# Kernel optimization log

Measured on AMD Instinct MI355X. Metric: run time of the kernel, lower is better.

Reference implementation:

```python
import jax, jax.numpy as jnp
import numpy as np

D_MODEL = 1024
NUM_HEADS = 16
HEAD_DIM = D_MODEL // NUM_HEADS
SCALE = HEAD_DIM ** -0.5


def setup_inputs() -> dict:
    key = jax.random.key(0)
    ks = jax.random.split(key, 8)
    B, Nq, Nk = 2, 2048, 2048
    s = D_MODEL ** -0.5  # init scale for weights
    return {
        "query": jax.random.normal(ks[0], (B, Nq, D_MODEL), jnp.float32),
        "key": jax.random.normal(ks[1], (B, Nk, D_MODEL), jnp.float32),
        "value": jax.random.normal(ks[2], (B, Nk, D_MODEL), jnp.float32),
        "Wq": jax.random.normal(ks[3], (D_MODEL, D_MODEL), jnp.float32) * s,
        "Wk": jax.random.normal(ks[4], (D_MODEL, D_MODEL), jnp.float32) * s,
        "Wv": jax.random.normal(ks[5], (D_MODEL, D_MODEL), jnp.float32) * s,
        "Wo": jax.random.normal(ks[6], (D_MODEL, D_MODEL), jnp.float32) * s,
        "bo": jnp.zeros((D_MODEL,), jnp.float32),
    }


def reference(query, key, value, Wq, Wk, Wv, Wo, bo):
    B, Nq, C = query.shape
    Nk = key.shape[1]
    H, Dh = NUM_HEADS, HEAD_DIM
    # projections (torch Linear: x @ W.T)
    q = (query @ Wq.T).reshape(B, Nq, H, Dh).transpose(0, 2, 1, 3)  # [B,H,Nq,Dh]
    k = (key @ Wk.T).reshape(B, Nk, H, Dh).transpose(0, 2, 1, 3)    # [B,H,Nk,Dh]
    v = (value @ Wv.T).reshape(B, Nk, H, Dh).transpose(0, 2, 1, 3)  # [B,H,Nk,Dh]
    # explicit attention: QK^T * scale -> softmax -> @V
    sim = jnp.einsum("bhqd,bhkd->bhqk", q, k) * SCALE
    attn = jax.nn.softmax(sim, axis=-1)
    out = jnp.einsum("bhqk,bhkd->bhqd", attn, v)
    out = out.transpose(0, 2, 1, 3).reshape(B, Nq, C)
    return out @ Wo.T + bo
```

## Files before the change

### kernel.cpp

```cpp
#include <hip/hip_runtime.h>
#include <hip/hip_bf16.h>

typedef __attribute__((ext_vector_type(8))) short short8;
typedef __attribute__((ext_vector_type(4))) short short4v;
typedef __attribute__((ext_vector_type(4))) float f32x4;

#define DEVFN static __device__ __forceinline__

constexpr int D_MODEL = 1024;
constexpr int NH  = 16;
constexpr int DH  = 64;
constexpr int SEQ = 2048;
constexpr float SCALE_LOG2E = 0.125f * 1.44269504088896341f;

DEVFN short bf16s(float f) {
  __hip_bfloat16 h = __float2bfloat16(f);
  short s; __builtin_memcpy(&s, &h, 2);
  return s;
}

DEVFN float fast_exp2(float x) {
#if __has_builtin(__builtin_amdgcn_exp2f)
  return __builtin_amdgcn_exp2f(x);
#else
  return exp2f(x);
#endif
}

DEVFN void gload_lds16(const void* g, void* l) {
  __builtin_amdgcn_global_load_lds(
      (const __attribute__((address_space(1))) unsigned int*)g,
      (__attribute__((address_space(3))) unsigned int*)l, 16, 0, 0);
}

__global__ __launch_bounds__(256)
void castk(const float* __restrict__ src, short* __restrict__ dst, int n8, float scale)
{
  int i = blockIdx.x * blockDim.x + threadIdx.x;
  if (i >= n8) return;
  const float4 a = *(const float4*)(src + (size_t)i*8);
  const float4 b = *(const float4*)(src + (size_t)i*8 + 4);
  short8 v;
  v[0]=bf16s(a.x*scale); v[1]=bf16s(a.y*scale); v[2]=bf16s(a.z*scale); v[3]=bf16s(a.w*scale);
  v[4]=bf16s(b.x*scale); v[5]=bf16s(b.y*scale); v[6]=bf16s(b.z*scale); v[7]=bf16s(b.w*scale);
  *(short8*)(dst + (size_t)i*8) = v;
}

__global__ __launch_bounds__(256, 3)
void qkv_gemm(const float* __restrict__ Aq, const float* __restrict__ Ak,
              const float* __restrict__ Av,
              const short* __restrict__ Wq, const short* __restrict__ Wk,
              const short* __restrict__ Wv,
              short* __restrict__ Qp, short* __restrict__ Kp, short* __restrict__ Vp)
{
  __shared__ char smem[16384 + 8192];
  char* AsB = smem;
  char* WsB = smem + 16384;

  const int z = blockIdx.z;
  const float* Af = (z == 0) ? Aq : (z == 1) ? Ak : Av;
  const short* Wb = (z == 0) ? Wq : (z == 1) ? Wk : Wv;
  short* Cp       = (z == 0) ? Qp : (z == 1) ? Kp : Vp;

  const int tid = threadIdx.x, lane = tid & 63, w = tid >> 6;
  const int wr = w >> 1, wc = w & 1;
  const int l15 = lane & 15, l4 = lane >> 4;
  const int m0 = blockIdx.y * 128, n0 = blockIdx.x * 128;

  f32x4 acc[4][4];
  #pragma unroll
  for (int i = 0; i < 4; ++i)
    #pragma unroll
    for (int j = 0; j < 4; ++j) acc[i][j] = f32x4{0.f,0.f,0.f,0.f};

  for (int kt = 0; kt < D_MODEL/32; ++kt) {
    const int k0 = kt * 32;
    #pragma unroll
    for (int p = 0; p < 4; ++p) {
      const int off = (w*4 + p)*1024 + lane*16;
      const int row = off >> 7;
      const int cb  = (off & 127) ^ ((row & 7) << 4);
      gload_lds16(Af + (size_t)(m0 + row)*D_MODEL + k0 + (cb >> 2),
                  AsB + (w*4 + p)*1024);
    }
    #pragma unroll
    for (int p = 0; p < 2; ++p) {
      const int off = (w*2 + p)*1024 + lane*16;
      const int row = off >> 6;
      const int cb  = (off & 63) ^ ((row & 3) << 4);
      gload_lds16(Wb + (size_t)(n0 + row)*D_MODEL + k0 + (cb >> 1),
                  WsB + (w*2 + p)*1024);
    }
    __syncthreads();

    short8 af[4], bf[4];
    #pragma unroll
    for (int fi = 0; fi < 4; ++fi) {
      const int row = wr*64 + fi*16 + l15;
      const int s_ = (row & 7) << 4;
      f32x4 x0 = *(const f32x4*)(AsB + row*128 + ((l4*32) ^ s_));
      f32x4 x1 = *(const f32x4*)(AsB + row*128 + ((l4*32 + 16) ^ s_));
      short8 a;
      a[0]=bf16s(x0[0]); a[1]=bf16s(x0[1]); a[2]=bf16s(x0[2]); a[3]=bf16s(x0[3]);
      a[4]=bf16s(x1[0]); a[5]=bf16s(x1[1]); a[6]=bf16s(x1[2]); a[7]=bf16s(x1[3]);
      af[fi] = a;
    }
    #pragma unroll
    for (int fj = 0; fj < 4; ++fj) {
      const int row = wc*64 + fj*16 + l15;
      bf[fj] = *(const short8*)(WsB + row*64 + ((l4*16) ^ ((row & 3) << 4)));
    }
    #pragma unroll
    for (int fi = 0; fi < 4; ++fi)
      #pragma unroll
      for (int fj = 0; fj < 4; ++fj)
        acc[fi][fj] = __builtin_amdgcn_mfma_f32_16x16x32_bf16(af[fi], bf[fj], acc[fi][fj], 0, 0, 0);
    __syncthreads();
  }

  #pragma unroll
  for (int fi = 0; fi < 4; ++fi)
    #pragma unroll
    for (int fj = 0; fj < 4; ++fj)
      #pragma unroll
      for (int r = 0; r < 4; ++r) {
        const int m = m0 + wr*64 + fi*16 + l4*4 + r;
        const int j = n0 + wc*64 + fj*16 + l15;
        const int b = m >> 11, n = m & (SEQ-1);
        const int h = j >> 6,  d = j & 63;
        const short v = bf16s(acc[fi][fj][r]);
        if (z == 2)
          Cp[((size_t)(b*NH + h)*DH + d)*SEQ + n] = v;
        else
          Cp[(((size_t)(b*NH + h)*SEQ + n) << 6) + d] = v;
      }
}

__global__ __launch_bounds__(256, 4)
void gemm_out(const short* __restrict__ A, const short* __restrict__ Wb,
              const float* __restrict__ bias, float* __restrict__ Cp)
{
  __shared__ char smem[8192 + 4096];
  char* AsB = smem;
  char* WsB = smem + 8192;

  const int tid = threadIdx.x, lane = tid & 63, w = tid >> 6;
  const int wr = w >> 1, wc = w & 1;
  const int l15 = lane & 15, l4 = lane >> 4;
  const int m0 = blockIdx.y * 128, n0 = blockIdx.x * 64;

  f32x4 acc[4][2];
  #pragma unroll
  for (int i = 0; i < 4; ++i)
    #pragma unroll
    for (int j = 0; j < 2; ++j) acc[i][j] = f32x4{0.f,0.f,0.f,0.f};

  for (int kt = 0; kt < D_MODEL/32; ++kt) {
    const int k0 = kt * 32;
    #pragma unroll
    for (int p = 0; p < 2; ++p) {
      const int off = (w*2 + p)*1024 + lane*16;
      const int row = off >> 6;
      const int cb  = (off & 63) ^ ((row & 3) << 4);
      gload_lds16(A + (size_t)(m0 + row)*D_MODEL + k0 + (cb >> 1),
                  AsB + (w*2 + p)*1024);
    }
    {
      const int off = w*1024 + lane*16;
      const int row = off >> 6;
      const int cb  = (off & 63) ^ ((row & 3) << 4);
      gload_lds16(Wb + (size_t)(n0 + row)*D_MODEL + k0 + (cb >> 1),
                  WsB + w*1024);
    }
    __syncthreads();

    short8 af[4], bf[2];
    #pragma unroll
    for (int fi = 0; fi < 4; ++fi) {
      const int row = wr*64 + fi*16 + l15;
      af[fi] = *(const short8*)(AsB + row*64 + ((l4*16) ^ ((row & 3) << 4)));
    }
    #pragma unroll
    for (int fj = 0; fj < 2; ++fj) {
      const int row = wc*32 + fj*16 + l15;
      bf[fj] = *(const short8*)(WsB + row*64 + ((l4*16) ^ ((row & 3) << 4)));
    }
    #pragma unroll
    for (int fi = 0; fi < 4; ++fi)
      #pragma unroll
      for (int fj = 0; fj < 2; ++fj)
        acc[fi][fj] = __builtin_amdgcn_mfma_f32_16x16x32_bf16(af[fi], bf[fj], acc[fi][fj], 0, 0, 0);
    __syncthreads();
  }

  float bj[2];
  #pragma unroll
  for (int fj = 0; fj < 2; ++fj) bj[fj] = bias[n0 + wc*32 + fj*16 + l15];
  #pragma unroll
  for (int fi = 0; fi < 4; ++fi)
    #pragma unroll
    for (int fj = 0; fj < 2; ++fj)
      #pragma unroll
      for (int r = 0; r < 4; ++r) {
        const int m = m0 + wr*64 + fi*16 + l4*4 + r;
        const int j = n0 + wc*32 + fj*16 + l15;
        Cp[(size_t)m*D_MODEL + j] = acc[fi][fj][r] + bj[fj];
      }
}

__global__ __launch_bounds__(512, 2)
void attn_fwd(const short* __restrict__ Qh, const short* __restrict__ Kh,
              const short* __restrict__ Vt, __hip_bfloat16* __restrict__ AO)
{
  __shared__ char smem[49152];
  char* PsAll = smem + 32768;

  const int tid = threadIdx.x, lane = tid & 63, w = tid >> 6;
  const int l15 = lane & 15, l4 = lane >> 4;
  const int bh = blockIdx.y, q0 = blockIdx.x * 128;
  const int b = bh >> 4, h = bh & 15;
  const size_t base = (size_t)bh * SEQ * DH;
  char* PsB = PsAll + w * 2048;

  const short* Kg = Kh + base;
  const short* Vg = Vt + base;

  short8 qf[2];
  #pragma unroll
  for (int kc = 0; kc < 2; ++kc)
    qf[kc] = *(const short8*)(Qh + base + (size_t)(q0 + w*16 + l15)*DH + kc*32 + l4*8);

  float m = -1e30f, l = 0.f;
  f32x4 o[4];
  #pragma unroll
  for (int fj = 0; fj < 4; ++fj) o[fj] = f32x4{0.f,0.f,0.f,0.f};

  const int srow = tid >> 3, sco = tid & 7;
  const int sdst = (srow*128 + sco*16) ^ ((srow & 7) << 4);

  short8 kr = *(const short8*)(Kg + (size_t)srow*DH + sco*8);
  short8 vr = *(const short8*)(Vg + (size_t)srow*SEQ + sco*8);
  *(short8*)(smem + sdst) = kr;
  *(short8*)(smem + 8192 + sdst) = vr;
  __syncthreads();

  constexpr int NT = SEQ/64;
  for (int kt = 0; kt < NT; ++kt) {
    const int cur = kt & 1;
    char* KsB = smem + cur*16384;
    char* VsB = KsB + 8192;

    if (kt + 1 < NT) {
      kr = *(const short8*)(Kg + (size_t)((kt+1)*64 + srow)*DH + sco*8);
      vr = *(const short8*)(Vg + (size_t)srow*SEQ + (kt+1)*64 + sco*8);
    }

    f32x4 s[4];
    #pragma unroll
    for (int fj = 0; fj < 4; ++fj) s[fj] = f32x4{0.f,0.f,0.f,0.f};
    #pragma unroll
    for (int kc = 0; kc < 2; ++kc)
      #pragma unroll
      for (int fj = 0; fj < 4; ++fj) {
        const int row = fj*16 + l15;
        short8 kf = *(const short8*)(KsB + ((row*128 + (kc*32 + l4*8)*2) ^ ((row & 7) << 4)));
        s[fj] = __builtin_amdgcn_mfma_f32_16x16x32_bf16(kf, qf[kc], s[fj], 0, 0, 0);
      }

    float pmax = s[0][0];
    #pragma unroll
    for (int fj = 0; fj < 4; ++fj)
      #pragma unroll
      for (int r = 0; r < 4; ++r) pmax = fmaxf(pmax, s[fj][r]);
    pmax = fmaxf(pmax, __shfl_xor(pmax, 16, 64));
    pmax = fmaxf(pmax, __shfl_xor(pmax, 32, 64));
    const float mn = fmaxf(m, pmax);
    const float al = fast_exp2(m - mn);
    m = mn;
    float rs = 0.f;
    #pragma unroll
    for (int fj = 0; fj < 4; ++fj)
      #pragma unroll
      for (int r = 0; r < 4; ++r) {
        s[fj][r] = fast_exp2(s[fj][r] - m);
        rs += s[fj][r];
      }
    rs += __shfl_xor(rs, 16, 64);
    rs += __shfl_xor(rs, 32, 64);
    l = l * al + rs;

    #pragma unroll
    for (int fj = 0; fj < 4; ++fj) {
      short4v c;
      c[0]=bf16s(s[fj][0]); c[1]=bf16s(s[fj][1]); c[2]=bf16s(s[fj][2]); c[3]=bf16s(s[fj][3]);
      const int byo = (l15*128 + (fj*16 + l4*4)*2) ^ ((l15 & 7) << 4);
      *(short4v*)(PsB + byo) = c;
    }

    float alr[4];
    #pragma unroll
    for (int r = 0; r < 4; ++r) alr[r] = __shfl(al, l4*4 + r, 64);
    #pragma unroll
    for (int fj = 0; fj < 4; ++fj)
      #pragma unroll
      for (int r = 0; r < 4; ++r) o[fj][r] *= alr[r];

    #pragma unroll
    for (int kc = 0; kc < 2; ++kc) {
      const int pb = (l15*128 + (kc*32 + l4*8)*2) ^ ((l15 & 7) << 4);
      short8 pa = *(const short8*)(PsB + pb);
      #pragma unroll
      for (int fj = 0; fj < 4; ++fj) {
        const int row = fj*16 + l15;
        short8 vf = *(const short8*)(VsB + ((row*128 + (kc*32 + l4*8)*2) ^ ((row & 7) << 4)));
        o[fj] = __builtin_amdgcn_mfma_f32_16x16x32_bf16(pa, vf, o[fj], 0, 0, 0);
      }
    }

    if (kt + 1 < NT) {
      char* KnB = smem + (cur ^ 1)*16384;
      *(short8*)(KnB + sdst) = kr;
      *(short8*)(KnB + 8192 + sdst) = vr;
    }
    __syncthreads();
  }

  const float inv = 1.0f / l;
  float ivr[4];
  #pragma unroll
  for (int r = 0; r < 4; ++r) ivr[r] = __shfl(inv, l4*4 + r, 64);
  #pragma unroll
  for (int fj = 0; fj < 4; ++fj)
    #pragma unroll
    for (int r = 0; r < 4; ++r) {
      const int n = q0 + w*16 + l4*4 + r;
      const int d = h*64 + fj*16 + l15;
      AO[(size_t)(b*SEQ + n)*D_MODEL + d] = __float2bfloat16(o[fj][r] * ivr[r]);
    }
}

extern "C" void kernel_launch(void* const* d_in, const int* in_sizes, int n_in,
                              void* d_out, int out_size, void* d_ws, size_t ws_size,
                              hipStream_t stream)
{
  const float* query = (const float*)d_in[0];
  const float* key_  = (const float*)d_in[1];
  const float* value = (const float*)d_in[2];
  const float* Wq = (const float*)d_in[3];
  const float* Wk = (const float*)d_in[4];
  const float* Wv = (const float*)d_in[5];
  const float* Wo = (const float*)d_in[6];
  const float* bo = (const float*)d_in[7];

  char* wsb = (char*)d_ws;
  short* Qp  = (short*)(wsb);
  short* Kp  = (short*)(wsb + (8u  << 20));
  short* Vp  = (short*)(wsb + (16u << 20));
  short* Wqb = (short*)(wsb + (24u << 20));
  short* Wkb = (short*)(wsb + (26u << 20));
  short* Wvb = (short*)(wsb + (28u << 20));
  short* Ao  = (short*)(wsb + (24u << 20));
  short* Wob = (short*)(wsb);

  const int nW = D_MODEL*D_MODEL/8;
  castk<<<nW/256, 256, 0, stream>>>(Wq, Wqb, nW, SCALE_LOG2E);
  castk<<<nW/256, 256, 0, stream>>>(Wk, Wkb, nW, 1.f);
  castk<<<nW/256, 256, 0, stream>>>(Wv, Wvb, nW, 1.f);

  dim3 gq(D_MODEL/128, (2*SEQ)/128, 3);
  qkv_gemm<<<gq, 256, 0, stream>>>(query, key_, value, Wqb, Wkb, Wvb, Qp, Kp, Vp);

  dim3 ga(SEQ/128, 2*NH);
  attn_fwd<<<ga, 512, 0, stream>>>(Qp, Kp, Vp, (__hip_bfloat16*)Ao);

  castk<<<nW/256, 256, 0, stream>>>(Wo, Wob, nW, 1.f);
  dim3 go(D_MODEL/64, (2*SEQ)/128);
  gemm_out<<<go, 256, 0, stream>>>(Ao, Wob, bo, (float*)d_out);
}
```

Measured before the change: 254.3 us.

## Double-buffer LDS with async global_load_lds and swizzle block-to-XCD mapping

After: 242.7 us. -4.5%, faster.

```diff
diff --git a/kernel.cpp b/kernel.cpp
--- a/kernel.cpp
+++ b/kernel.cpp
@@ -26,6 +26,8 @@
   return exp2f(x);
 #endif
 }
+
+DEVFN void wait_vm0() { asm volatile("s_waitcnt vmcnt(0)" ::: "memory"); }
 
 DEVFN void gload_lds16(const void* g, void* l) {
   __builtin_amdgcn_global_load_lds(
@@ -53,11 +55,14 @@
               const short* __restrict__ Wv,
               short* __restrict__ Qp, short* __restrict__ Kp, short* __restrict__ Vp)
 {
-  __shared__ char smem[16384 + 8192];
-  char* AsB = smem;
-  char* WsB = smem + 16384;
-
-  const int z = blockIdx.z;
+  __shared__ char smem[2*24576];
+
+  const int id  = blockIdx.x;
+  const int swz = (id & 7)*96 + (id >> 3);
+  const int z   = swz >> 8;
+  const int rr  = swz & 255;
+  const int m0  = (rr >> 3) * 128, n0 = (rr & 7) * 128;
+
   const float* Af = (z == 0) ? Aq : (z == 1) ? Ak : Av;
   const short* Wb = (z == 0) ? Wq : (z == 1) ? Wk : Wv;
   short* Cp       = (z == 0) ? Qp : (z == 1) ? Kp : Vp;
@@ -65,7 +70,6 @@
   const int tid = threadIdx.x, lane = tid & 63, w = tid >> 6;
   const int wr = w >> 1, wc = w & 1;
   const int l15 = lane & 15, l4 = lane >> 4;
-  const int m0 = blockIdx.y * 128, n0 = blockIdx.x * 128;
 
   f32x4 acc[4][4];
   #pragma unroll
@@ -73,15 +77,14 @@
     #pragma unroll
     for (int j = 0; j < 4; ++j) acc[i][j] = f32x4{0.f,0.f,0.f,0.f};
 
-  for (int kt = 0; kt < D_MODEL/32; ++kt) {
-    const int k0 = kt * 32;
+  auto stage = [&](char* buf, int k0) {
     #pragma unroll
     for (int p = 0; p < 4; ++p) {
       const int off = (w*4 + p)*1024 + lane*16;
       const int row = off >> 7;
       const int cb  = (off & 127) ^ ((row & 7) << 4);
       gload_lds16(Af + (size_t)(m0 + row)*D_MODEL + k0 + (cb >> 2),
-                  AsB + (w*4 + p)*1024);
+                  buf + (w*4 + p)*1024);
     }
     #pragma unroll
     for (int p = 0; p < 2; ++p) {
@@ -89,10 +92,19 @@
       const int row = off >> 6;
       const int cb  = (off & 63) ^ ((row & 3) << 4);
       gload_lds16(Wb + (size_t)(n0 + row)*D_MODEL + k0 + (cb >> 1),
-                  WsB + (w*2 + p)*1024);
-    }
-    __syncthreads();
-
+                  buf + 16384 + (w*2 + p)*1024);
+    }
+  };
+
+  stage(smem, 0);
+  wait_vm0();
+  __builtin_amdgcn_s_barrier();
+
+  for (int kt = 0; kt < D_MODEL/32; ++kt) {
+    char* buf = smem + (kt & 1)*24576;
+    if (kt + 1 < D_MODEL/32) stage(smem + ((kt+1) & 1)*24576, (kt+1)*32);
+
+    char* AsB = buf; char* WsB = buf + 16384;
     short8 af[4], bf[4];
     #pragma unroll
     for (int fi = 0; fi < 4; ++fi) {
@@ -115,7 +127,9 @@
       #pragma unroll
       for (int fj = 0; fj < 4; ++fj)
         acc[fi][fj] = __builtin_amdgcn_mfma_f32_16x16x32_bf16(af[fi], bf[fj], acc[fi][fj], 0, 0, 0);
-    __syncthreads();
+
+    wait_vm0();
+    __builtin_amdgcn_s_barrier();
   }
 
   #pragma unroll
@@ -140,14 +154,15 @@
 void gemm_out(const short* __restrict__ A, const short* __restrict__ Wb,
               const float* __restrict__ bias, float* __restrict__ Cp)
 {
-  __shared__ char smem[8192 + 4096];
-  char* AsB = smem;
-  char* WsB = smem + 8192;
+  __shared__ char smem[2*12288];
+
+  const int id  = blockIdx.x;
+  const int swz = (id & 7)*64 + (id >> 3);
+  const int m0  = (swz >> 4) * 128, n0 = (swz & 15) * 64;
 
   const int tid = threadIdx.x, lane = tid & 63, w = tid >> 6;
   const int wr = w >> 1, wc = w & 1;
   const int l15 = lane & 15, l4 = lane >> 4;
-  const int m0 = blockIdx.y * 128, n0 = blockIdx.x * 64;
 
   f32x4 acc[4][2];
   #pragma unroll
@@ -155,25 +170,33 @@
     #pragma unroll
     for (int j = 0; j < 2; ++j) acc[i][j] = f32x4{0.f,0.f,0.f,0.f};
 
-  for (int kt = 0; kt < D_MODEL/32; ++kt) {
-    const int k0 = kt * 32;
+  auto stage = [&](char* buf, int k0) {
     #pragma unroll
     for (int p = 0; p < 2; ++p) {
       const int off = (w*2 + p)*1024 + lane*16;
       const int row = off >> 6;
       const int cb  = (off & 63) ^ ((row & 3) << 4);
       gload_lds16(A + (size_t)(m0 + row)*D_MODEL + k0 + (cb >> 1),
-                  AsB + (w*2 + p)*1024);
+                  buf + (w*2 + p)*1024);
     }
     {
       const int off = w*1024 + lane*16;
       const int row = off >> 6;
       const int cb  = (off & 63) ^ ((row & 3) << 4);
       gload_lds16(Wb + (size_t)(n0 + row)*D_MODEL + k0 + (cb >> 1),
-                  WsB + w*1024);
-    }
-    __syncthreads();
-
+                  buf + 8192 + w*1024);
+    }
+  };
+
+  stage(smem, 0);
+  wait_vm0();
+  __builtin_amdgcn_s_barrier();
+
+  for (int kt = 0; kt < D_MODEL/32; ++kt) {
+    char* buf = smem + (kt & 1)*12288;
+    if (kt + 1 < D_MODEL/32) stage(smem + ((kt+1) & 1)*12288, (kt+1)*32);
+
+    char* AsB = buf; char* WsB = buf + 8192;
     short8 af[4], bf[2];
     #pragma unroll
     for (int fi = 0; fi < 4; ++fi) {
@@ -190,7 +213,9 @@
       #pragma unroll
       for (int fj = 0; fj < 2; ++fj)
         acc[fi][fj] = __builtin_amdgcn_mfma_f32_16x16x32_bf16(af[fi], bf[fj], acc[fi][fj], 0, 0, 0);
-    __syncthreads();
+
+    wait_vm0();
+    __builtin_amdgcn_s_barrier();
   }
 
   float bj[2];
@@ -212,12 +237,16 @@
 void attn_fwd(const short* __restrict__ Qh, const short* __restrict__ Kh,
               const short* __restrict__ Vt, __hip_bfloat16* __restrict__ AO)
 {
-  __shared__ char smem[49152];
+  __shared__ char smem[2*16384 + 16384];
   char* PsAll = smem + 32768;
+
+  const int id  = blockIdx.x;
+  const int swz = (id & 7)*64 + (id >> 3);
+  const int bh  = swz >> 4;
+  const int q0  = (swz & 15) * 128;
 
   const int tid = threadIdx.x, lane = tid & 63, w = tid >> 6;
   const int l15 = lane & 15, l4 = lane >> 4;
-  const int bh = blockIdx.y, q0 = blockIdx.x * 128;
   const int b = bh >> 4, h = bh & 15;
   const size_t base = (size_t)bh * SEQ * DH;
   char* PsB = PsAll + w * 2048;
@@ -235,25 +264,24 @@
   #pragma unroll
   for (int fj = 0; fj < 4; ++fj) o[fj] = f32x4{0.f,0.f,0.f,0.f};
 
-  const int srow = tid >> 3, sco = tid & 7;
-  const int sdst = (srow*128 + sco*16) ^ ((srow & 7) << 4);
-
-  short8 kr = *(const short8*)(Kg + (size_t)srow*DH + sco*8);
-  short8 vr = *(const short8*)(Vg + (size_t)srow*SEQ + sco*8);
-  *(short8*)(smem + sdst) = kr;
-  *(short8*)(smem + 8192 + sdst) = vr;
-  __syncthreads();
+  const int soff = w*1024 + lane*16;
+  const int srow = soff >> 7;
+  const int scb  = (soff & 127) ^ ((srow & 7) << 4);
+
+  auto stage = [&](char* buf, int kt) {
+    gload_lds16(Kg + (size_t)(kt*64 + srow)*DH + (scb >> 1), buf + w*1024);
+    gload_lds16(Vg + (size_t)srow*SEQ + kt*64 + (scb >> 1),  buf + 8192 + w*1024);
+  };
+
+  stage(smem, 0);
+  wait_vm0();
+  __builtin_amdgcn_s_barrier();
 
   constexpr int NT = SEQ/64;
   for (int kt = 0; kt < NT; ++kt) {
-    const int cur = kt & 1;
-    char* KsB = smem + cur*16384;
+    char* KsB = smem + (kt & 1)*16384;
     char* VsB = KsB + 8192;
-
-    if (kt + 1 < NT) {
-      kr = *(const short8*)(Kg + (size_t)((kt+1)*64 + srow)*DH + sco*8);
-      vr = *(const short8*)(Vg + (size_t)srow*SEQ + (kt+1)*64 + sco*8);
-    }
+    if (kt + 1 < NT) stage(smem + ((kt+1) & 1)*16384, kt + 1);
 
     f32x4 s[4];
     #pragma unroll
@@ -317,12 +345,8 @@
       }
     }
 
-    if (kt + 1 < NT) {
-      char* KnB = smem + (cur ^ 1)*16384;
-      *(short8*)(KnB + sdst) = kr;
-      *(short8*)(KnB + 8192 + sdst) = vr;
-    }
-    __syncthreads();
+    wait_vm0();
+    __builtin_amdgcn_s_barrier();
   }
 
   const float inv = 1.0f / l;
@@ -367,13 +391,9 @@
   castk<<<nW/256, 256, 0, stream>>>(Wk, Wkb, nW, 1.f);
   castk<<<nW/256, 256, 0, stream>>>(Wv, Wvb, nW, 1.f);
 
-  dim3 gq(D_MODEL/128, (2*SEQ)/128, 3);
-  qkv_gemm<<<gq, 256, 0, stream>>>(query, key_, value, Wqb, Wkb, Wvb, Qp, Kp, Vp);
-
-  dim3 ga(SEQ/128, 2*NH);
-  attn_fwd<<<ga, 512, 0, stream>>>(Qp, Kp, Vp, (__hip_bfloat16*)Ao);
+  qkv_gemm<<<768, 256, 0, stream>>>(query, key_, value, Wqb, Wkb, Wvb, Qp, Kp, Vp);
+  attn_fwd<<<512, 512, 0, stream>>>(Qp, Kp, Vp, (__hip_bfloat16*)Ao);
 
   castk<<<nW/256, 256, 0, stream>>>(Wo, Wob, nW, 1.f);
-  dim3 go(D_MODEL/64, (2*SEQ)/128);
-  gemm_out<<<go, 256, 0, stream>>>(Ao, Wob, bo, (float*)d_out);
-}
+  gemm_out<<<512, 256, 0, stream>>>(Ao, Wob, bo, (float*)d_out);
+}
```
